# Kernel tuning notes

Hardware: AMD Instinct MI355X
Metric: run time of the kernel (lower is better)

Reference implementation:

```python
import jax, jax.numpy as jnp
import numpy as np
from jax import lax

RADIUS = 8
EPS = 1e-3
EPS_LOG = 1e-6
EPS_SCALE = 1e-4
A_COMP = 0.7
B_SHIFT = 0.0
DETAIL_GAIN = 1.0
DOWN = 0.5
# detail_threshold=0 and target_mean=0 -> those branches are inactive (defaults)

DN = (('NCHW', 'OIHW', 'NCHW'))


def _box_filter(x4d):
    """Separable box filter on [1,1,H,W] with reflect padding, kernel 2r+1."""
    k = 2 * RADIUS + 1
    xp = jnp.pad(x4d, ((0, 0), (0, 0), (RADIUS, RADIUS), (RADIUS, RADIUS)), mode='reflect')
    kh = jnp.full((1, 1, 1, k), 1.0 / k, dtype=x4d.dtype)
    kv = jnp.full((1, 1, k, 1), 1.0 / k, dtype=x4d.dtype)
    y = lax.conv_general_dilated(xp, kh, (1, 1), 'VALID', dimension_numbers=DN)
    y = lax.conv_general_dilated(y, kv, (1, 1), 'VALID', dimension_numbers=DN)
    return y


def _guided_filter(img):
    """Self-guided filter on a 2D image [H, W]."""
    x4 = img[None, None]
    mean_I = _box_filter(x4)
    mean_II = _box_filter(x4 * x4)
    var_I = mean_II - mean_I * mean_I
    a = var_I / (var_I + EPS)
    b = mean_I - a * mean_I
    out = _box_filter(a) * x4 + _box_filter(b)
    return out[0, 0]


def _bilinear_resize(img, oh, ow):
    """Bilinear resize [H,W] -> [oh,ow], half-pixel centers (align_corners=False),
    no antialias, matching torch F.interpolate(mode='bilinear')."""
    H, W = img.shape
    ys = jnp.maximum((jnp.arange(oh, dtype=img.dtype) + 0.5) * (H / oh) - 0.5, 0.0)
    xs = jnp.maximum((jnp.arange(ow, dtype=img.dtype) + 0.5) * (W / ow) - 0.5, 0.0)
    y0 = jnp.floor(ys)
    x0 = jnp.floor(xs)
    wy = (ys - y0)[:, None]
    wx = (xs - x0)[None, :]
    y0i = jnp.clip(y0.astype(jnp.int32), 0, H - 1)
    y1i = jnp.minimum(y0i + 1, H - 1)
    x0i = jnp.clip(x0.astype(jnp.int32), 0, W - 1)
    x1i = jnp.minimum(x0i + 1, W - 1)
    # vertical lerp, then horizontal lerp (separable)
    vert = img[y0i, :] * (1.0 - wy) + img[y1i, :] * wy       # [oh, W]
    out = vert[:, x0i] * (1.0 - wx) + vert[:, x1i] * wx      # [oh, ow]
    return out


def setup_inputs() -> dict:
    key = jax.random.key(0)
    x = jax.random.uniform(key, (2160, 3840, 3), dtype=jnp.float32)
    return {"x": x}


def reference(x) -> jnp.ndarray:
    H, W = x.shape[0], x.shape[1]
    Y = 0.2126 * x[..., 0] + 0.7152 * x[..., 1] + 0.0722 * x[..., 2]
    Y_log = jnp.log2(jnp.maximum(Y, EPS_LOG))
    # fast path: downsample -> guided filter -> upsample
    dh, dw = int(H * DOWN), int(W * DOWN)
    Y_log_down = _bilinear_resize(Y_log, dh, dw)
    Y_base_down = _guided_filter(Y_log_down)
    Y_base = _bilinear_resize(Y_base_down, H, W)
    Y_detail = Y_log - Y_base  # detail_threshold=0 -> no suppression
    Y_tm = (A_COMP * Y_base + B_SHIFT) + DETAIL_GAIN * Y_detail
    Y_out = jnp.exp2(Y_tm)
    scale = Y_out / (Y + EPS_SCALE)
    out = jnp.clip(x * scale[..., None], 0.0, 1.0)
    # target_mean=0 -> no global mean rescale
    return out
```

## Files before the change

### kernel.cpp

```cpp
#include <hip/hip_runtime.h>
#include <math.h>

#define H_FULL 2160
#define W_FULL 3840
#define H_D    1080
#define W_D    1920
#define KLEN   17
#define INV_K2 (1.0f/289.0f)

#if __has_builtin(__builtin_amdgcn_logf)
#define FAST_LOG2(x) __builtin_amdgcn_logf(x)
#else
#define FAST_LOG2(x) log2f(x)
#endif
#if __has_builtin(__builtin_amdgcn_exp2f)
#define FAST_EXP2(x) __builtin_amdgcn_exp2f(x)
#else
#define FAST_EXP2(x) exp2f(x)
#endif
#if __has_builtin(__builtin_amdgcn_rcpf)
#define FAST_RCP(x) __builtin_amdgcn_rcpf(x)
#else
#define FAST_RCP(x) (1.0f/(x))
#endif

static __device__ __forceinline__ int refl(int i, int n) {
    if (i < 0) i = -i;
    else if (i >= n) i = 2*n - 2 - i;
    return i;
}
static __device__ __forceinline__ float lum(float r, float g, float b) {
    return 0.2126f*r + 0.7152f*g + 0.0722f*b;
}
static __device__ __forceinline__ float lg(float y) {
    return FAST_LOG2(fmaxf(y, 1e-6f));
}

__global__ __launch_bounds__(256) void k_down(const float* __restrict__ x,
                                              float* __restrict__ I) {
    int t = blockIdx.x * 256 + threadIdx.x;
    int p = t * 2;
    int i = p / W_D;
    int j = p - i * W_D;
    const float4* r0 = (const float4*)(x + ((size_t)(2*i)   * W_FULL + 2*j) * 3);
    const float4* r1 = (const float4*)(x + ((size_t)(2*i+1) * W_FULL + 2*j) * 3);
    float4 a0 = r0[0], a1 = r0[1], a2 = r0[2];
    float4 b0 = r1[0], b1 = r1[1], b2 = r1[2];
    float y00 = lum(a0.x,a0.y,a0.z), y01 = lum(a0.w,a1.x,a1.y);
    float y02 = lum(a1.z,a1.w,a2.x), y03 = lum(a2.y,a2.z,a2.w);
    float y10 = lum(b0.x,b0.y,b0.z), y11 = lum(b0.w,b1.x,b1.y);
    float y12 = lum(b1.z,b1.w,b2.x), y13 = lum(b2.y,b2.z,b2.w);
    float o0 = 0.25f * (lg(y00)+lg(y01)+lg(y10)+lg(y11));
    float o1 = 0.25f * (lg(y02)+lg(y03)+lg(y12)+lg(y13));
    *(float2*)(I + (size_t)i * W_D + j) = make_float2(o0, o1);
}

__global__ __launch_bounds__(512, 6) void k_fused(const float* __restrict__ I,
                                                  const float* __restrict__ x,
                                                  float* __restrict__ out) {
    __shared__ char lds[52088];
    float*  sIc   = (float*) (lds);
    float*  sIf   = (float*) (lds + 4760);
    float2* ab    = (float2*)(lds + 4760);
    float2* hI    = (float2*)(lds + 25160);
    float2* hab   = (float2*)(lds + 25160);
    float*  baseL = (float*) (lds + 39160);

    int tx0 = blockIdx.x * 32;
    int ty0 = blockIdx.y * 32;
    int tid = threadIdx.x;

    for (int e = tid; e < 66 * 66; e += 512) {
        int r = e / 66, c = e - r * 66;
        sIf[r * 67 + c] =
            I[(size_t)refl(ty0 - 17 + r, H_D) * W_D + refl(tx0 - 17 + c, W_D)];
    }
    __syncthreads();

    if (tid < 330) {
        int r = tid / 5, run = tid - (tid / 5) * 5;
        int c0 = run * 10;
        const float* p = &sIf[r * 67 + c0];
        float s1 = 0.f, s2 = 0.f;
        #pragma unroll
        for (int k = 0; k < KLEN; ++k) { float v = p[k]; s1 += v; s2 += v * v; }
        float2* o = &hI[r * 51 + c0];
        o[0] = make_float2(s1, s2);
        #pragma unroll
        for (int m = 1; m < 10; ++m) {
            float vo = p[m - 1], vi = p[m + 16];
            s1 += vi - vo;
            s2 += vi * vi - vo * vo;
            o[m] = make_float2(s1, s2);
        }
    }
    for (int e = tid; e < 34 * 34; e += 512) {
        int r = e / 34, c = e - r * 34;
        sIc[r * 35 + c] = sIf[(r + 16) * 67 + (c + 16)];
    }
    __syncthreads();

    if (tid < 250) {
        int c = tid % 50, run = tid / 50;
        int r0 = run * 10;
        const float2* p = &hI[r0 * 51 + c];
        float s1 = 0.f, s2 = 0.f;
        #pragma unroll
        for (int k = 0; k < KLEN; ++k) { float2 v = p[k * 51]; s1 += v.x; s2 += v.y; }
        float2* o = &ab[r0 * 51 + c];
        #pragma unroll
        for (int m = 0; m < 10; ++m) {
            if (m) {
                float2 vi = p[(m + 16) * 51], vo = p[(m - 1) * 51];
                s1 += vi.x - vo.x;
                s2 += vi.y - vo.y;
            }
            float mI  = s1 * INV_K2;
            float mII = s2 * INV_K2;
            float var = mII - mI * mI;
            float av  = var / (var + 1e-3f);
            o[m * 51] = make_float2(av, mI - av * mI);
        }
    }
    __syncthreads();

    if (tid < 200) {
        int r = tid % 50, run = tid / 50;
        int c0  = (run < 2) ? run * 9 : 18 + (run - 2) * 8;
        int len = (run < 2) ? 9 : 8;
        const float2* p = &ab[r * 51 + c0];
        float sa = 0.f, sb = 0.f;
        #pragma unroll
        for (int k = 0; k < KLEN; ++k) { float2 v = p[k]; sa += v.x; sb += v.y; }
        float2* o = &hab[r * 35 + c0];
        o[0] = make_float2(sa, sb);
        #pragma unroll
        for (int m = 1; m < 9; ++m) {
            if (m < len) {
                float2 vi = p[m + 16], vo = p[m - 1];
                sa += vi.x - vo.x;
                sb += vi.y - vo.y;
                o[m] = make_float2(sa, sb);
            }
        }
    }
    __syncthreads();

    if (tid < 136) {
        int cc = tid % 34, run = tid / 34;
        int r0  = (run < 2) ? run * 9 : 18 + (run - 2) * 8;
        int len = (run < 2) ? 9 : 8;
        const float2* p = &hab[r0 * 35 + cc];
        float sa = 0.f, sb = 0.f;
        #pragma unroll
        for (int k = 0; k < KLEN; ++k) { float2 v = p[k * 35]; sa += v.x; sb += v.y; }
        #pragma unroll
        for (int m = 0; m < 9; ++m) {
            if (m < len) {
                if (m) {
                    float2 vi = p[(m + 16) * 35], vo = p[(m - 1) * 35];
                    sa += vi.x - vo.x;
                    sb += vi.y - vo.y;
                }
                int br = r0 + m;
                baseL[br * 35 + cc] =
                    (sa * INV_K2) * sIc[br * 35 + cc] + sb * INV_K2;
            }
        }
    }
    __syncthreads();

    int q  = tid & 15;
    int r  = tid >> 4;
    int j0 = tx0 * 2 + q * 4;
    int gc0 = tx0 + 2 * q - 1;
    int l0 = max(gc0, 0) - (tx0 - 1);
    int l1 = 2 * q + 1, l2 = 2 * q + 2;
    int l3 = min(gc0 + 3, W_D - 1) - (tx0 - 1);

    #pragma unroll
    for (int s = 0; s < 2; ++s) {
        int oy = ty0 * 2 + r + s * 32;
        if (oy < H_FULL) {
            int y0g = (oy - 1) >> 1;
            int ly0 = max(y0g, 0) - (ty0 - 1);
            int ly1 = min(y0g + 1, H_D - 1) - (ty0 - 1);
            float wy = (oy & 1) ? 0.25f : 0.75f;
            const float* b0r = &baseL[ly0 * 35];
            const float* b1r = &baseL[ly1 * 35];
            float v0 = b0r[l0] + (b1r[l0] - b0r[l0]) * wy;
            float v1 = b0r[l1] + (b1r[l1] - b0r[l1]) * wy;
            float v2 = b0r[l2] + (b1r[l2] - b0r[l2]) * wy;
            float v3 = b0r[l3] + (b1r[l3] - b0r[l3]) * wy;
            float Yb[4];
            Yb[0] = v0 + (v1 - v0) * 0.75f;
            Yb[1] = v1 + (v2 - v1) * 0.25f;
            Yb[2] = v1 + (v2 - v1) * 0.75f;
            Yb[3] = v2 + (v3 - v2) * 0.25f;

            size_t off = ((size_t)oy * W_FULL + j0) * 3;
            const float4* px = (const float4*)(x + off);
            float4 q0 = px[0], q1 = px[1], q2 = px[2];
            float rgb[12] = {q0.x,q0.y,q0.z,q0.w, q1.x,q1.y,q1.z,q1.w, q2.x,q2.y,q2.z,q2.w};
            float res[12];
            #pragma unroll
            for (int k = 0; k < 4; ++k) {
                float rr = rgb[3*k], gg = rgb[3*k+1], bb = rgb[3*k+2];
                float Y = lum(rr, gg, bb);
                float sc = fmaxf(Y, 1e-6f) * FAST_EXP2(-0.3f * Yb[k]) * FAST_RCP(Y + 1e-4f);
                res[3*k]   = fminf(fmaxf(rr * sc, 0.f), 1.f);
                res[3*k+1] = fminf(fmaxf(gg * sc, 0.f), 1.f);
                res[3*k+2] = fminf(fmaxf(bb * sc, 0.f), 1.f);
            }
            float4* po = (float4*)(out + off);
            po[0] = make_float4(res[0], res[1], res[2],  res[3]);
            po[1] = make_float4(res[4], res[5], res[6],  res[7]);
            po[2] = make_float4(res[8], res[9], res[10], res[11]);
        }
    }
}

extern "C" void kernel_launch(void* const* d_in, const int* in_sizes, int n_in,
                              void* d_out, int out_size, void* d_ws, size_t ws_size,
                              hipStream_t stream) {
    (void)in_sizes; (void)n_in; (void)out_size; (void)ws_size;
    const float* x = (const float*)d_in[0];
    float* out = (float*)d_out;
    float* I = (float*)d_ws;

    k_down <<<dim3(4050, 1, 1), dim3(256, 1, 1), 0, stream>>>(x, I);
    k_fused<<<dim3(60, 34, 1),  dim3(512, 1, 1), 0, stream>>>(I, x, out);
}
```

Measured before the change: 69.83 us.

## Split fused filter+tonemap into separate filter and streaming tonemap kernels

Splits the fused kernel in two. The first writes the half-res guided-filter base to a workspace plane, and the second is a separate full-res elementwise tonemap kernel that reads x, the base and writes out. The aim is to decouple the LDS-heavy, low-occupancy filter from the bandwidth-bound tonemap, so the streaming pass runs with full occupancy and the filter tiles do less. The cost is an extra launch plus a round trip of the base plane through global memory. The old fused path remains as a fallback when the workspace is too small.

```diff
diff --git a/kernel.cpp b/kernel.cpp
--- a/kernel.cpp
+++ b/kernel.cpp
@@ -53,6 +53,178 @@
     float o0 = 0.25f * (lg(y00)+lg(y01)+lg(y10)+lg(y11));
     float o1 = 0.25f * (lg(y02)+lg(y03)+lg(y12)+lg(y13));
     *(float2*)(I + (size_t)i * W_D + j) = make_float2(o0, o1);
+}
+
+__global__ __launch_bounds__(512, 6) void k_filter(const float* __restrict__ I,
+                                                   float* __restrict__ base) {
+    __shared__ char lds[52088];
+    float*  sIc   = (float*) (lds);
+    float*  sIf   = (float*) (lds + 4760);
+    float2* ab    = (float2*)(lds + 4760);
+    float2* hI    = (float2*)(lds + 25160);
+    float2* hab   = (float2*)(lds + 25160);
+    float*  baseL = (float*) (lds + 39160);
+
+    int tx0 = blockIdx.x * 32;
+    int ty0 = blockIdx.y * 32;
+    int tid = threadIdx.x;
+
+    for (int e = tid; e < 66 * 66; e += 512) {
+        int r = e / 66, c = e - r * 66;
+        sIf[r * 67 + c] =
+            I[(size_t)refl(ty0 - 17 + r, H_D) * W_D + refl(tx0 - 17 + c, W_D)];
+    }
+    __syncthreads();
+
+    if (tid < 330) {
+        int r = tid / 5, run = tid - (tid / 5) * 5;
+        int c0 = run * 10;
+        const float* p = &sIf[r * 67 + c0];
+        float s1 = 0.f, s2 = 0.f;
+        #pragma unroll
+        for (int k = 0; k < KLEN; ++k) { float v = p[k]; s1 += v; s2 += v * v; }
+        float2* o = &hI[r * 51 + c0];
+        o[0] = make_float2(s1, s2);
+        #pragma unroll
+        for (int m = 1; m < 10; ++m) {
+            float vo = p[m - 1], vi = p[m + 16];
+            s1 += vi - vo;
+            s2 += vi * vi - vo * vo;
+            o[m] = make_float2(s1, s2);
+        }
+    }
+    for (int e = tid; e < 34 * 34; e += 512) {
+        int r = e / 34, c = e - r * 34;
+        sIc[r * 35 + c] = sIf[(r + 16) * 67 + (c + 16)];
+    }
+    __syncthreads();
+
+    if (tid < 250) {
+        int c = tid % 50, run = tid / 50;
+        int r0 = run * 10;
+        const float2* p = &hI[r0 * 51 + c];
+        float s1 = 0.f, s2 = 0.f;
+        #pragma unroll
+        for (int k = 0; k < KLEN; ++k) { float2 v = p[k * 51]; s1 += v.x; s2 += v.y; }
+        float2* o = &ab[r0 * 51 + c];
+        #pragma unroll
+        for (int m = 0; m < 10; ++m) {
+            if (m) {
+                float2 vi = p[(m + 16) * 51], vo = p[(m - 1) * 51];
+                s1 += vi.x - vo.x;
+                s2 += vi.y - vo.y;
+            }
+            float mI  = s1 * INV_K2;
+            float mII = s2 * INV_K2;
+            float var = mII - mI * mI;
+            float av  = var / (var + 1e-3f);
+            o[m * 51] = make_float2(av, mI - av * mI);
+        }
+    }
+    __syncthreads();
+
+    if (tid < 200) {
+        int r = tid % 50, run = tid / 50;
+        int c0  = (run < 2) ? run * 9 : 18 + (run - 2) * 8;
+        int len = (run < 2) ? 9 : 8;
+        const float2* p = &ab[r * 51 + c0];
+        float sa = 0.f, sb = 0.f;
+        #pragma unroll
+        for (int k = 0; k < KLEN; ++k) { float2 v = p[k]; sa += v.x; sb += v.y; }
+        float2* o = &hab[r * 35 + c0];
+        o[0] = make_float2(sa, sb);
+        #pragma unroll
+        for (int m = 1; m < 9; ++m) {
+            if (m < len) {
+                float2 vi = p[m + 16], vo = p[m - 1];
+                sa += vi.x - vo.x;
+                sb += vi.y - vo.y;
+                o[m] = make_float2(sa, sb);
+            }
+        }
+    }
+    __syncthreads();
+
+    if (tid < 136) {
+        int cc = tid % 34, run = tid / 34;
+        int r0  = (run < 2) ? run * 9 : 18 + (run - 2) * 8;
+        int len = (run < 2) ? 9 : 8;
+        const float2* p = &hab[r0 * 35 + cc];
+        float sa = 0.f, sb = 0.f;
+        #pragma unroll
+        for (int k = 0; k < KLEN; ++k) { float2 v = p[k * 35]; sa += v.x; sb += v.y; }
+        #pragma unroll
+        for (int m = 0; m < 9; ++m) {
+            if (m < len) {
+                if (m) {
+                    float2 vi = p[(m + 16) * 35], vo = p[(m - 1) * 35];
+                    sa += vi.x - vo.x;
+                    sb += vi.y - vo.y;
+                }
+                int br = r0 + m;
+                baseL[br * 35 + cc] =
+                    (sa * INV_K2) * sIc[br * 35 + cc] + sb * INV_K2;
+            }
+        }
+    }
+    __syncthreads();
+
+    for (int e = tid; e < 32 * 32; e += 512) {
+        int r = e >> 5, c = e & 31;
+        int gr = ty0 + r;
+        if (gr < H_D) base[(size_t)gr * W_D + (tx0 + c)] = baseL[(r + 1) * 35 + (c + 1)];
+    }
+}
+
+__global__ __launch_bounds__(256) void k_tm(const float* __restrict__ x,
+                                            const float* __restrict__ base,
+                                            float* __restrict__ out) {
+    int t = blockIdx.x * 256 + threadIdx.x;
+    int oy = t / 960;
+    int g  = t - oy * 960;
+    int j0 = g * 4;
+    int k2 = g * 2;
+
+    int y0g = (oy - 1) >> 1;
+    int y0 = max(y0g, 0);
+    int y1 = min(y0g + 1, H_D - 1);
+    float wy = (oy & 1) ? 0.25f : 0.75f;
+    const float* b0 = base + (size_t)y0 * W_D;
+    const float* b1 = base + (size_t)y1 * W_D;
+    int c0 = max(k2 - 1, 0);
+    int c3 = min(k2 + 2, W_D - 1);
+    float u0 = b0[c0],     w0 = b1[c0];
+    float u1 = b0[k2],     w1 = b1[k2];
+    float u2 = b0[k2 + 1], w2 = b1[k2 + 1];
+    float u3 = b0[c3],     w3 = b1[c3];
+    float v0 = u0 + (w0 - u0) * wy;
+    float v1 = u1 + (w1 - u1) * wy;
+    float v2 = u2 + (w2 - u2) * wy;
+    float v3 = u3 + (w3 - u3) * wy;
+    float Yb[4];
+    Yb[0] = v0 + (v1 - v0) * 0.75f;
+    Yb[1] = v1 + (v2 - v1) * 0.25f;
+    Yb[2] = v1 + (v2 - v1) * 0.75f;
+    Yb[3] = v2 + (v3 - v2) * 0.25f;
+
+    size_t off = ((size_t)oy * W_FULL + j0) * 3;
+    const float4* px = (const float4*)(x + off);
+    float4 q0 = px[0], q1 = px[1], q2 = px[2];
+    float rgb[12] = {q0.x,q0.y,q0.z,q0.w, q1.x,q1.y,q1.z,q1.w, q2.x,q2.y,q2.z,q2.w};
+    float res[12];
+    #pragma unroll
+    for (int k = 0; k < 4; ++k) {
+        float rr = rgb[3*k], gg = rgb[3*k+1], bb = rgb[3*k+2];
+        float Y = lum(rr, gg, bb);
+        float sc = fmaxf(Y, 1e-6f) * FAST_EXP2(-0.3f * Yb[k]) * FAST_RCP(Y + 1e-4f);
+        res[3*k]   = fminf(fmaxf(rr * sc, 0.f), 1.f);
+        res[3*k+1] = fminf(fmaxf(gg * sc, 0.f), 1.f);
+        res[3*k+2] = fminf(fmaxf(bb * sc, 0.f), 1.f);
+    }
+    float4* po = (float4*)(out + off);
+    po[0] = make_float4(res[0], res[1], res[2],  res[3]);
+    po[1] = make_float4(res[4], res[5], res[6],  res[7]);
+    po[2] = make_float4(res[8], res[9], res[10], res[11]);
 }
 
 __global__ __launch_bounds__(512, 6) void k_fused(const float* __restrict__ I,
@@ -223,11 +395,19 @@
 extern "C" void kernel_launch(void* const* d_in, const int* in_sizes, int n_in,
                               void* d_out, int out_size, void* d_ws, size_t ws_size,
                               hipStream_t stream) {
-    (void)in_sizes; (void)n_in; (void)out_size; (void)ws_size;
+    (void)in_sizes; (void)n_in; (void)out_size;
     const float* x = (const float*)d_in[0];
     float* out = (float*)d_out;
     float* I = (float*)d_ws;
-
-    k_down <<<dim3(4050, 1, 1), dim3(256, 1, 1), 0, stream>>>(x, I);
-    k_fused<<<dim3(60, 34, 1),  dim3(512, 1, 1), 0, stream>>>(I, x, out);
-}
+    size_t plane = (size_t)H_D * W_D;
+
+    if (ws_size >= 2 * plane * sizeof(float)) {
+        float* base = I + plane;
+        k_down  <<<dim3(4050, 1, 1), dim3(256, 1, 1), 0, stream>>>(x, I);
+        k_filter<<<dim3(60, 34, 1),  dim3(512, 1, 1), 0, stream>>>(I, base);
+        k_tm    <<<dim3(8100, 1, 1), dim3(256, 1, 1), 0, stream>>>(x, base, out);
+    } else {
+        k_down  <<<dim3(4050, 1, 1), dim3(256, 1, 1), 0, stream>>>(x, I);
+        k_fused <<<dim3(60, 34, 1),  dim3(512, 1, 1), 0, stream>>>(I, x, out);
+    }
+}
```

Measured after the change: 80.48 us. 15.3% more time.

## Drop shared input tile, read halo from global, split ab stage to shrink LDS

Applied to the files above, without the earlier changes.

Removes the 66x66 shared staging of the downsampled image. The horizontal pass now reads I straight from global/L1, reflecting columns only for edge blocks. The ab computation is split into two phases writing to aliased buffers, which shrinks LDS from about 52KB to about 39KB and raises launch bounds to 8 blocks per CU for higher occupancy. The center values for the base reconstruction are reloaded from global. The cost is more global loads that are less well coalesced and one extra barrier.

```diff
diff --git a/kernel.cpp b/kernel.cpp
--- a/kernel.cpp
+++ b/kernel.cpp
@@ -55,61 +55,64 @@
     *(float2*)(I + (size_t)i * W_D + j) = make_float2(o0, o1);
 }
 
-__global__ __launch_bounds__(512, 6) void k_fused(const float* __restrict__ I,
-                                                  const float* __restrict__ x,
-                                                  float* __restrict__ out) {
-    __shared__ char lds[52088];
-    float*  sIc   = (float*) (lds);
-    float*  sIf   = (float*) (lds + 4760);
-    float2* ab    = (float2*)(lds + 4760);
-    float2* hI    = (float2*)(lds + 25160);
-    float2* hab   = (float2*)(lds + 25160);
-    float*  baseL = (float*) (lds + 39160);
+__global__ __launch_bounds__(512, 8) void k_fused4(const float* __restrict__ I,
+                                                   const float* __restrict__ x,
+                                                   float* __restrict__ out) {
+    __shared__ char lds[38928];
+    float2* abLo  = (float2*)(lds);
+    float*  baseL = (float*) (lds);
+    float2* hI    = (float2*)(lds + 12000);
+    float2* abHi  = (float2*)(lds + 12000);
+    float2* hab   = (float2*)(lds + 20000);
 
     int tx0 = blockIdx.x * 32;
     int ty0 = blockIdx.y * 32;
     int tid = threadIdx.x;
-
-    for (int e = tid; e < 66 * 66; e += 512) {
-        int r = e / 66, c = e - r * 66;
-        sIf[r * 67 + c] =
-            I[(size_t)refl(ty0 - 17 + r, H_D) * W_D + refl(tx0 - 17 + c, W_D)];
-    }
-    __syncthreads();
+    bool xedge = (tx0 < 17) || (tx0 > W_D - 51);
 
     if (tid < 330) {
         int r = tid / 5, run = tid - (tid / 5) * 5;
         int c0 = run * 10;
-        const float* p = &sIf[r * 67 + c0];
+        int grow = refl(ty0 - 17 + r, H_D);
+        const float* gI = I + (size_t)grow * W_D;
+        int gc = tx0 - 17 + c0;
+        float keep[9];
         float s1 = 0.f, s2 = 0.f;
         #pragma unroll
-        for (int k = 0; k < KLEN; ++k) { float v = p[k]; s1 += v; s2 += v * v; }
+        for (int k = 0; k < 9; ++k) {
+            int col = gc + k; if (xedge) col = refl(col, W_D);
+            float v = gI[col];
+            keep[k] = v; s1 += v; s2 += v * v;
+        }
+        #pragma unroll
+        for (int k = 9; k < 17; ++k) {
+            int col = gc + k; if (xedge) col = refl(col, W_D);
+            float v = gI[col];
+            s1 += v; s2 += v * v;
+        }
         float2* o = &hI[r * 51 + c0];
         o[0] = make_float2(s1, s2);
         #pragma unroll
         for (int m = 1; m < 10; ++m) {
-            float vo = p[m - 1], vi = p[m + 16];
+            int col = gc + m + 16; if (xedge) col = refl(col, W_D);
+            float vi = gI[col];
+            float vo = keep[m - 1];
             s1 += vi - vo;
             s2 += vi * vi - vo * vo;
             o[m] = make_float2(s1, s2);
         }
     }
-    for (int e = tid; e < 34 * 34; e += 512) {
-        int r = e / 34, c = e - r * 34;
-        sIc[r * 35 + c] = sIf[(r + 16) * 67 + (c + 16)];
-    }
     __syncthreads();
 
     if (tid < 250) {
         int c = tid % 50, run = tid / 50;
-        int r0 = run * 10;
+        int r0 = run * 6;
         const float2* p = &hI[r0 * 51 + c];
         float s1 = 0.f, s2 = 0.f;
         #pragma unroll
         for (int k = 0; k < KLEN; ++k) { float2 v = p[k * 51]; s1 += v.x; s2 += v.y; }
-        float2* o = &ab[r0 * 51 + c];
-        #pragma unroll
-        for (int m = 0; m < 10; ++m) {
+        #pragma unroll
+        for (int m = 0; m < 6; ++m) {
             if (m) {
                 float2 vi = p[(m + 16) * 51], vo = p[(m - 1) * 51];
                 s1 += vi.x - vo.x;
@@ -119,20 +122,44 @@
             float mII = s2 * INV_K2;
             float var = mII - mI * mI;
             float av  = var / (var + 1e-3f);
-            o[m * 51] = make_float2(av, mI - av * mI);
+            abLo[(r0 + m) * 50 + c] = make_float2(av, mI - av * mI);
+        }
+    }
+    __syncthreads();
+
+    if (tid < 250) {
+        int c = tid % 50, run = tid / 50;
+        int r0 = 30 + run * 4;
+        const float2* p = &hI[r0 * 51 + c];
+        float s1 = 0.f, s2 = 0.f;
+        #pragma unroll
+        for (int k = 0; k < KLEN; ++k) { float2 v = p[k * 51]; s1 += v.x; s2 += v.y; }
+        #pragma unroll
+        for (int m = 0; m < 4; ++m) {
+            if (m) {
+                float2 vi = p[(m + 16) * 51], vo = p[(m - 1) * 51];
+                s1 += vi.x - vo.x;
+                s2 += vi.y - vo.y;
+            }
+            float mI  = s1 * INV_K2;
+            float mII = s2 * INV_K2;
+            float var = mII - mI * mI;
+            float av  = var / (var + 1e-3f);
+            abHi[(r0 + m - 30) * 50 + c] = make_float2(av, mI - av * mI);
         }
     }
     __syncthreads();
 
     if (tid < 200) {
-        int r = tid % 50, run = tid / 50;
+        int rr = tid % 50, run = tid / 50;
         int c0  = (run < 2) ? run * 9 : 18 + (run - 2) * 8;
         int len = (run < 2) ? 9 : 8;
-        const float2* p = &ab[r * 51 + c0];
+        const float2* row = (rr < 30) ? &abLo[rr * 50] : &abHi[(rr - 30) * 50];
+        const float2* p = row + c0;
         float sa = 0.f, sb = 0.f;
         #pragma unroll
         for (int k = 0; k < KLEN; ++k) { float2 v = p[k]; sa += v.x; sb += v.y; }
-        float2* o = &hab[r * 35 + c0];
+        float2* o = &hab[rr * 35 + c0];
         o[0] = make_float2(sa, sb);
         #pragma unroll
         for (int m = 1; m < 9; ++m) {
@@ -150,6 +177,9 @@
         int cc = tid % 34, run = tid / 34;
         int r0  = (run < 2) ? run * 9 : 18 + (run - 2) * 8;
         int len = (run < 2) ? 9 : 8;
+        int gcol = tx0 - 1 + cc;
+        if (gcol < 0) gcol = -gcol;
+        else if (gcol >= W_D) gcol = 2 * W_D - 2 - gcol;
         const float2* p = &hab[r0 * 35 + cc];
         float sa = 0.f, sb = 0.f;
         #pragma unroll
@@ -163,8 +193,9 @@
                     sb += vi.y - vo.y;
                 }
                 int br = r0 + m;
-                baseL[br * 35 + cc] =
-                    (sa * INV_K2) * sIc[br * 35 + cc] + sb * INV_K2;
+                int grow = refl(ty0 - 1 + br, H_D);
+                float Ic = I[(size_t)grow * W_D + gcol];
+                baseL[br * 35 + cc] = (sa * INV_K2) * Ic + sb * INV_K2;
             }
         }
     }
@@ -228,6 +259,6 @@
     float* out = (float*)d_out;
     float* I = (float*)d_ws;
 
-    k_down <<<dim3(4050, 1, 1), dim3(256, 1, 1), 0, stream>>>(x, I);
-    k_fused<<<dim3(60, 34, 1),  dim3(512, 1, 1), 0, stream>>>(I, x, out);
-}
+    k_down  <<<dim3(4050, 1, 1), dim3(256, 1, 1), 0, stream>>>(x, I);
+    k_fused4<<<dim3(60, 34, 1),  dim3(512, 1, 1), 0, stream>>>(I, x, out);
+}
```

After: 74.48 us. 1.07x slower.

## Process two tiles per block and overlap previous tile's output with filter stages

Applied to the files above, without the earlier changes.

Each block now handles two horizontally adjacent tiles. While the guided-filter stages of the second tile run, the threads left idle in each stage apply the tone map and write the full-resolution output of the first tile from the baseL it already holds. The aim is to fill idle lanes during the partially occupied box-filter phases and to hide global memory traffic behind LDS compute. The cost is more complex indexing, more registers held across barriers for the precomputed Yb values, and half as many blocks, which may reduce parallelism.

```diff
diff --git a/kernel.cpp b/kernel.cpp
--- a/kernel.cpp
+++ b/kernel.cpp
@@ -55,9 +55,62 @@
     *(float2*)(I + (size_t)i * W_D + j) = make_float2(o0, o1);
 }
 
-__global__ __launch_bounds__(512, 6) void k_fused(const float* __restrict__ I,
-                                                  const float* __restrict__ x,
-                                                  float* __restrict__ out) {
+static __device__ __forceinline__ float4 computeYb(int u, int ptx0, int pty0,
+                                                   const float* baseL) {
+    int s_ = u >> 9, rem = u & 511, r_ = rem >> 4, q_ = rem & 15;
+    int oy = pty0 * 2 + r_ + s_ * 32;
+    if (oy >= H_FULL) oy = H_FULL - 1;
+    int gc0 = ptx0 + 2 * q_ - 1;
+    int l0 = max(gc0, 0) - (ptx0 - 1);
+    int l1 = 2 * q_ + 1, l2 = 2 * q_ + 2;
+    int l3 = min(gc0 + 3, W_D - 1) - (ptx0 - 1);
+    int y0g = (oy - 1) >> 1;
+    int ly0 = max(y0g, 0) - (pty0 - 1);
+    int ly1 = min(y0g + 1, H_D - 1) - (pty0 - 1);
+    float wy = (oy & 1) ? 0.25f : 0.75f;
+    const float* b0r = &baseL[ly0 * 35];
+    const float* b1r = &baseL[ly1 * 35];
+    float v0 = b0r[l0] + (b1r[l0] - b0r[l0]) * wy;
+    float v1 = b0r[l1] + (b1r[l1] - b0r[l1]) * wy;
+    float v2 = b0r[l2] + (b1r[l2] - b0r[l2]) * wy;
+    float v3 = b0r[l3] + (b1r[l3] - b0r[l3]) * wy;
+    return make_float4(v0 + (v1 - v0) * 0.75f,
+                       v1 + (v2 - v1) * 0.25f,
+                       v1 + (v2 - v1) * 0.75f,
+                       v2 + (v3 - v2) * 0.25f);
+}
+
+static __device__ __forceinline__ void doUnit(float4 Yb, int u, int ptx0, int pty0,
+                                              const float* __restrict__ x,
+                                              float* __restrict__ out) {
+    int s_ = u >> 9, rem = u & 511, r_ = rem >> 4, q_ = rem & 15;
+    int oy = pty0 * 2 + r_ + s_ * 32;
+    if (oy >= H_FULL) return;
+    int j0 = ptx0 * 2 + q_ * 4;
+    size_t off = ((size_t)oy * W_FULL + j0) * 3;
+    const float4* px = (const float4*)(x + off);
+    float4 q0 = px[0], q1 = px[1], q2 = px[2];
+    float rgb[12] = {q0.x,q0.y,q0.z,q0.w, q1.x,q1.y,q1.z,q1.w, q2.x,q2.y,q2.z,q2.w};
+    float Ybv[4] = {Yb.x, Yb.y, Yb.z, Yb.w};
+    float res[12];
+    #pragma unroll
+    for (int k = 0; k < 4; ++k) {
+        float rr = rgb[3*k], gg = rgb[3*k+1], bb = rgb[3*k+2];
+        float Y = lum(rr, gg, bb);
+        float sc = fmaxf(Y, 1e-6f) * FAST_EXP2(-0.3f * Ybv[k]) * FAST_RCP(Y + 1e-4f);
+        res[3*k]   = fminf(fmaxf(rr * sc, 0.f), 1.f);
+        res[3*k+1] = fminf(fmaxf(gg * sc, 0.f), 1.f);
+        res[3*k+2] = fminf(fmaxf(bb * sc, 0.f), 1.f);
+    }
+    float4* po = (float4*)(out + off);
+    po[0] = make_float4(res[0], res[1], res[2],  res[3]);
+    po[1] = make_float4(res[4], res[5], res[6],  res[7]);
+    po[2] = make_float4(res[8], res[9], res[10], res[11]);
+}
+
+__global__ __launch_bounds__(512, 6) void k_fused6(const float* __restrict__ I,
+                                                   const float* __restrict__ x,
+                                                   float* __restrict__ out) {
     __shared__ char lds[52088];
     float*  sIc   = (float*) (lds);
     float*  sIf   = (float*) (lds + 4760);
@@ -66,117 +119,140 @@
     float2* hab   = (float2*)(lds + 25160);
     float*  baseL = (float*) (lds + 39160);
 
-    int tx0 = blockIdx.x * 32;
     int ty0 = blockIdx.y * 32;
     int tid = threadIdx.x;
 
-    for (int e = tid; e < 66 * 66; e += 512) {
-        int r = e / 66, c = e - r * 66;
-        sIf[r * 67 + c] =
-            I[(size_t)refl(ty0 - 17 + r, H_D) * W_D + refl(tx0 - 17 + c, W_D)];
-    }
-    __syncthreads();
-
-    if (tid < 330) {
-        int r = tid / 5, run = tid - (tid / 5) * 5;
-        int c0 = run * 10;
-        const float* p = &sIf[r * 67 + c0];
-        float s1 = 0.f, s2 = 0.f;
-        #pragma unroll
-        for (int k = 0; k < KLEN; ++k) { float v = p[k]; s1 += v; s2 += v * v; }
-        float2* o = &hI[r * 51 + c0];
-        o[0] = make_float2(s1, s2);
-        #pragma unroll
-        for (int m = 1; m < 10; ++m) {
-            float vo = p[m - 1], vi = p[m + 16];
-            s1 += vi - vo;
-            s2 += vi * vi - vo * vo;
-            o[m] = make_float2(s1, s2);
-        }
-    }
-    for (int e = tid; e < 34 * 34; e += 512) {
-        int r = e / 34, c = e - r * 34;
-        sIc[r * 35 + c] = sIf[(r + 16) * 67 + (c + 16)];
-    }
-    __syncthreads();
-
-    if (tid < 250) {
-        int c = tid % 50, run = tid / 50;
-        int r0 = run * 10;
-        const float2* p = &hI[r0 * 51 + c];
-        float s1 = 0.f, s2 = 0.f;
-        #pragma unroll
-        for (int k = 0; k < KLEN; ++k) { float2 v = p[k * 51]; s1 += v.x; s2 += v.y; }
-        float2* o = &ab[r0 * 51 + c];
-        #pragma unroll
-        for (int m = 0; m < 10; ++m) {
-            if (m) {
-                float2 vi = p[(m + 16) * 51], vo = p[(m - 1) * 51];
-                s1 += vi.x - vo.x;
-                s2 += vi.y - vo.y;
-            }
-            float mI  = s1 * INV_K2;
-            float mII = s2 * INV_K2;
-            float var = mII - mI * mI;
-            float av  = var / (var + 1e-3f);
-            o[m * 51] = make_float2(av, mI - av * mI);
-        }
-    }
-    __syncthreads();
-
-    if (tid < 200) {
-        int r = tid % 50, run = tid / 50;
-        int c0  = (run < 2) ? run * 9 : 18 + (run - 2) * 8;
-        int len = (run < 2) ? 9 : 8;
-        const float2* p = &ab[r * 51 + c0];
-        float sa = 0.f, sb = 0.f;
-        #pragma unroll
-        for (int k = 0; k < KLEN; ++k) { float2 v = p[k]; sa += v.x; sb += v.y; }
-        float2* o = &hab[r * 35 + c0];
-        o[0] = make_float2(sa, sb);
-        #pragma unroll
-        for (int m = 1; m < 9; ++m) {
-            if (m < len) {
-                float2 vi = p[m + 16], vo = p[m - 1];
-                sa += vi.x - vo.x;
-                sb += vi.y - vo.y;
-                o[m] = make_float2(sa, sb);
-            }
-        }
-    }
-    __syncthreads();
-
-    if (tid < 136) {
-        int cc = tid % 34, run = tid / 34;
-        int r0  = (run < 2) ? run * 9 : 18 + (run - 2) * 8;
-        int len = (run < 2) ? 9 : 8;
-        const float2* p = &hab[r0 * 35 + cc];
-        float sa = 0.f, sb = 0.f;
-        #pragma unroll
-        for (int k = 0; k < KLEN; ++k) { float2 v = p[k * 35]; sa += v.x; sb += v.y; }
-        #pragma unroll
-        for (int m = 0; m < 9; ++m) {
-            if (m < len) {
+    float4 YbA = make_float4(0.f,0.f,0.f,0.f);
+    float4 YbB = YbA, YbC = YbA, YbD = YbA;
+
+    #pragma unroll
+    for (int k = 0; k < 2; ++k) {
+        int tx0  = (blockIdx.x * 2 + k) * 32;
+        int ptx0 = (blockIdx.x * 2 + k - 1) * 32;
+
+        if (k == 1) {
+            if (tid >= 330)              YbA = computeYb(tid - 330,       ptx0, ty0, baseL);
+            if (tid >= 250)              YbB = computeYb(182 + tid - 250, ptx0, ty0, baseL);
+            if (tid >= 200)              YbC = computeYb(444 + tid - 200, ptx0, ty0, baseL);
+            if (tid >= 136 && tid < 404) YbD = computeYb(756 + tid - 136, ptx0, ty0, baseL);
+        }
+        for (int e = tid; e < 66 * 66; e += 512) {
+            int r = e / 66, c = e - r * 66;
+            sIf[r * 67 + c] =
+                I[(size_t)refl(ty0 - 17 + r, H_D) * W_D + refl(tx0 - 17 + c, W_D)];
+        }
+        __syncthreads();
+
+        if (tid < 330) {
+            int r = tid / 5, run = tid - (tid / 5) * 5;
+            int c0 = run * 10;
+            const float* p = &sIf[r * 67 + c0];
+            float s1 = 0.f, s2 = 0.f;
+            #pragma unroll
+            for (int kk = 0; kk < KLEN; ++kk) { float v = p[kk]; s1 += v; s2 += v * v; }
+            float2* o = &hI[r * 51 + c0];
+            o[0] = make_float2(s1, s2);
+            #pragma unroll
+            for (int m = 1; m < 10; ++m) {
+                float vo = p[m - 1], vi = p[m + 16];
+                s1 += vi - vo;
+                s2 += vi * vi - vo * vo;
+                o[m] = make_float2(s1, s2);
+            }
+        } else if (k == 1) {
+            doUnit(YbA, tid - 330, ptx0, ty0, x, out);
+        }
+        for (int e = tid; e < 34 * 34; e += 512) {
+            int r = e / 34, c = e - r * 34;
+            sIc[r * 35 + c] = sIf[(r + 16) * 67 + (c + 16)];
+        }
+        __syncthreads();
+
+        if (tid < 250) {
+            int c = tid % 50, run = tid / 50;
+            int r0 = run * 10;
+            const float2* p = &hI[r0 * 51 + c];
+            float s1 = 0.f, s2 = 0.f;
+            #pragma unroll
+            for (int kk = 0; kk < KLEN; ++kk) { float2 v = p[kk * 51]; s1 += v.x; s2 += v.y; }
+            float2* o = &ab[r0 * 51 + c];
+            #pragma unroll
+            for (int m = 0; m < 10; ++m) {
                 if (m) {
-                    float2 vi = p[(m + 16) * 35], vo = p[(m - 1) * 35];
+                    float2 vi = p[(m + 16) * 51], vo = p[(m - 1) * 51];
+                    s1 += vi.x - vo.x;
+                    s2 += vi.y - vo.y;
+                }
+                float mI  = s1 * INV_K2;
+                float mII = s2 * INV_K2;
+                float var = mII - mI * mI;
+                float av  = var / (var + 1e-3f);
+                o[m * 51] = make_float2(av, mI - av * mI);
+            }
+        } else if (k == 1) {
+            doUnit(YbB, 182 + tid - 250, ptx0, ty0, x, out);
+        }
+        __syncthreads();
+
+        if (tid < 200) {
+            int r = tid % 50, run = tid / 50;
+            int c0  = (run < 2) ? run * 9 : 18 + (run - 2) * 8;
+            int len = (run < 2) ? 9 : 8;
+            const float2* p = &ab[r * 51 + c0];
+            float sa = 0.f, sb = 0.f;
+            #pragma unroll
+            for (int kk = 0; kk < KLEN; ++kk) { float2 v = p[kk]; sa += v.x; sb += v.y; }
+            float2* o = &hab[r * 35 + c0];
+            o[0] = make_float2(sa, sb);
+            #pragma unroll
+            for (int m = 1; m < 9; ++m) {
+                if (m < len) {
+                    float2 vi = p[m + 16], vo = p[m - 1];
                     sa += vi.x - vo.x;
                     sb += vi.y - vo.y;
+                    o[m] = make_float2(sa, sb);
                 }
-                int br = r0 + m;
-                baseL[br * 35 + cc] =
-                    (sa * INV_K2) * sIc[br * 35 + cc] + sb * INV_K2;
-            }
-        }
+            }
+        } else if (k == 1) {
+            doUnit(YbC, 444 + tid - 200, ptx0, ty0, x, out);
+        }
+        __syncthreads();
+
+        if (tid < 136) {
+            int cc = tid % 34, run = tid / 34;
+            int r0  = (run < 2) ? run * 9 : 18 + (run - 2) * 8;
+            int len = (run < 2) ? 9 : 8;
+            const float2* p = &hab[r0 * 35 + cc];
+            float sa = 0.f, sb = 0.f;
+            #pragma unroll
+            for (int kk = 0; kk < KLEN; ++kk) { float2 v = p[kk * 35]; sa += v.x; sb += v.y; }
+            #pragma unroll
+            for (int m = 0; m < 9; ++m) {
+                if (m < len) {
+                    if (m) {
+                        float2 vi = p[(m + 16) * 35], vo = p[(m - 1) * 35];
+                        sa += vi.x - vo.x;
+                        sb += vi.y - vo.y;
+                    }
+                    int br = r0 + m;
+                    baseL[br * 35 + cc] =
+                        (sa * INV_K2) * sIc[br * 35 + cc] + sb * INV_K2;
+                }
+            }
+        } else if (k == 1 && tid >= 136 && tid < 404) {
+            doUnit(YbD, 756 + tid - 136, ptx0, ty0, x, out);
+        }
+        __syncthreads();
     }
-    __syncthreads();
-
+
+    int tx1 = (blockIdx.x * 2 + 1) * 32;
     int q  = tid & 15;
     int r  = tid >> 4;
-    int j0 = tx0 * 2 + q * 4;
-    int gc0 = tx0 + 2 * q - 1;
-    int l0 = max(gc0, 0) - (tx0 - 1);
+    int j0 = tx1 * 2 + q * 4;
+    int gc0 = tx1 + 2 * q - 1;
+    int l0 = max(gc0, 0) - (tx1 - 1);
     int l1 = 2 * q + 1, l2 = 2 * q + 2;
-    int l3 = min(gc0 + 3, W_D - 1) - (tx0 - 1);
+    int l3 = min(gc0 + 3, W_D - 1) - (tx1 - 1);
 
     #pragma unroll
     for (int s = 0; s < 2; ++s) {
@@ -192,25 +268,24 @@
             float v1 = b0r[l1] + (b1r[l1] - b0r[l1]) * wy;
             float v2 = b0r[l2] + (b1r[l2] - b0r[l2]) * wy;
             float v3 = b0r[l3] + (b1r[l3] - b0r[l3]) * wy;
-            float Yb[4];
-            Yb[0] = v0 + (v1 - v0) * 0.75f;
-            Yb[1] = v1 + (v2 - v1) * 0.25f;
-            Yb[2] = v1 + (v2 - v1) * 0.75f;
-            Yb[3] = v2 + (v3 - v2) * 0.25f;
-
+            float4 Yb = make_float4(v0 + (v1 - v0) * 0.75f,
+                                    v1 + (v2 - v1) * 0.25f,
+                                    v1 + (v2 - v1) * 0.75f,
+                                    v2 + (v3 - v2) * 0.25f);
             size_t off = ((size_t)oy * W_FULL + j0) * 3;
             const float4* px = (const float4*)(x + off);
             float4 q0 = px[0], q1 = px[1], q2 = px[2];
             float rgb[12] = {q0.x,q0.y,q0.z,q0.w, q1.x,q1.y,q1.z,q1.w, q2.x,q2.y,q2.z,q2.w};
+            float Ybv[4] = {Yb.x, Yb.y, Yb.z, Yb.w};
             float res[12];
             #pragma unroll
-            for (int k = 0; k < 4; ++k) {
-                float rr = rgb[3*k], gg = rgb[3*k+1], bb = rgb[3*k+2];
+            for (int kk = 0; kk < 4; ++kk) {
+                float rr = rgb[3*kk], gg = rgb[3*kk+1], bb = rgb[3*kk+2];
                 float Y = lum(rr, gg, bb);
-                float sc = fmaxf(Y, 1e-6f) * FAST_EXP2(-0.3f * Yb[k]) * FAST_RCP(Y + 1e-4f);
-                res[3*k]   = fminf(fmaxf(rr * sc, 0.f), 1.f);
-                res[3*k+1] = fminf(fmaxf(gg * sc, 0.f), 1.f);
-                res[3*k+2] = fminf(fmaxf(bb * sc, 0.f), 1.f);
+                float sc = fmaxf(Y, 1e-6f) * FAST_EXP2(-0.3f * Ybv[kk]) * FAST_RCP(Y + 1e-4f);
+                res[3*kk]   = fminf(fmaxf(rr * sc, 0.f), 1.f);
+                res[3*kk+1] = fminf(fmaxf(gg * sc, 0.f), 1.f);
+                res[3*kk+2] = fminf(fmaxf(bb * sc, 0.f), 1.f);
             }
             float4* po = (float4*)(out + off);
             po[0] = make_float4(res[0], res[1], res[2],  res[3]);
@@ -228,6 +303,6 @@
     float* out = (float*)d_out;
     float* I = (float*)d_ws;
 
-    k_down <<<dim3(4050, 1, 1), dim3(256, 1, 1), 0, stream>>>(x, I);
-    k_fused<<<dim3(60, 34, 1),  dim3(512, 1, 1), 0, stream>>>(I, x, out);
-}
+    k_down  <<<dim3(4050, 1, 1), dim3(256, 1, 1), 0, stream>>>(x, I);
+    k_fused6<<<dim3(30, 34, 1),  dim3(512, 1, 1), 0, stream>>>(I, x, out);
+}
```

Result: slower. 71.35 us (+2.2%).
